# Kernel optimization log

Hardware: AMD Instinct MI355X
Metric: run time of the kernel (lower is better)

## Reference

```python
import jax, jax.numpy as jnp
import numpy as np

B, S, D, H = 2, 2048, 1024, 16
DK = D // H


def setup_inputs() -> dict:
    key = jax.random.key(0)
    ks = jax.random.split(key, 12)
    s = 1.0 / np.sqrt(D)
    return {
        "query": jax.random.normal(ks[0], (B, S, D), dtype=jnp.float32),
        "key": jax.random.normal(ks[1], (B, S, D), dtype=jnp.float32),
        "value": jax.random.normal(ks[2], (B, S, D), dtype=jnp.float32),
        "mask": jax.random.randint(ks[3], (B, 1, 1, S), 0, 2, dtype=jnp.int32),
        "wq": jax.random.normal(ks[4], (D, D), dtype=jnp.float32) * s,
        "bq": jnp.zeros((D,), dtype=jnp.float32),
        "wk": jax.random.normal(ks[5], (D, D), dtype=jnp.float32) * s,
        "bk": jnp.zeros((D,), dtype=jnp.float32),
        "wv": jax.random.normal(ks[6], (D, D), dtype=jnp.float32) * s,
        "bv": jnp.zeros((D,), dtype=jnp.float32),
        "wo": jax.random.normal(ks[7], (D, D), dtype=jnp.float32) * s,
        "bo": jnp.zeros((D,), dtype=jnp.float32),
    }


def reference(query, key, value, mask, wq, bq, wk, bk, wv, bv, wo, bo):
    b, s, d = query.shape
    # torch Linear: y = x @ W^T + b, then split heads -> [B, H, S, dk]
    def proj(x, w, bias):
        return (x @ w.T + bias).reshape(b, -1, H, DK).transpose(0, 2, 1, 3)

    q = proj(query, wq, bq)
    k = proj(key, wk, bk)
    v = proj(value, wv, bv)

    scores = jnp.einsum("bhqd,bhkd->bhqk", q, k) / jnp.sqrt(jnp.float32(DK))
    scores = jnp.where(mask == 0, jnp.float32(-1e9), scores)
    attn = jax.nn.softmax(scores, axis=-1)  # [B,H,S,S]
    x = jnp.einsum("bhqk,bhkd->bhqd", attn, v)
    x = x.transpose(0, 2, 1, 3).reshape(b, s, d)
    return x @ wo.T + bo
```

## Files before the change

kernel.cpp:

```cpp
#include <hip/hip_runtime.h>
#include <math.h>

#define B_  2
#define S_  2048
#define D_  1024
#define H_  16
#define DK_ 64

typedef unsigned short u16;
typedef unsigned int u32;
typedef __bf16 bf16x8 __attribute__((ext_vector_type(8)));
typedef float f32x4 __attribute__((ext_vector_type(4)));
typedef float f32x16 __attribute__((ext_vector_type(16)));
typedef u32 u32x2 __attribute__((ext_vector_type(2)));
typedef u32 u32x4 __attribute__((ext_vector_type(4)));

typedef const __attribute__((address_space(1))) void* gas1_t;
typedef __attribute__((address_space(3))) void* las3_t;

__device__ __forceinline__ void gload_lds16(const void* g, void* l) {
    __builtin_amdgcn_global_load_lds((gas1_t)g, (las3_t)l, 16, 0, 0);
}

__device__ __forceinline__ u16 f2bf(float f) {
    union { float f; unsigned u; } v; v.f = f;
    return (u16)((v.u + 0x7fffu + ((v.u >> 16) & 1u)) >> 16);
}

__device__ __forceinline__ u32 pack_bf16_2(float lo, float hi) {
    union { float f; u32 u; } a, b;
    a.f = lo; b.f = hi;
    return __builtin_amdgcn_perm(b.u + 0x8000u, a.u + 0x8000u, 0x07060302u);
}

__global__ __launch_bounds__(256)
void cast_all(const float* __restrict__ q, const float* __restrict__ k,
              const float* __restrict__ v, const float* __restrict__ wq,
              const float* __restrict__ wk, const float* __restrict__ wv,
              const float* __restrict__ wo, const int* __restrict__ mask,
              u16* __restrict__ qb, u16* __restrict__ kb, u16* __restrict__ vb,
              u16* __restrict__ wqb, u16* __restrict__ wkb, u16* __restrict__ wvb,
              u16* __restrict__ wob, float* __restrict__ mfac,
              float* __restrict__ nmaskf)
{
    const int bi = blockIdx.x;
    const int tid = threadIdx.x;
    if (bi >= 2064) {
        const int b = bi - 2064;
        __shared__ int red[256];
        int c = 0;
#pragma unroll
        for (int j = 0; j < 8; ++j)
            c += (mask[b * S_ + tid * 8 + j] == 0) ? 1 : 0;
        red[tid] = c;
        __syncthreads();
        for (int s = 128; s > 0; s >>= 1) {
            if (tid < s) red[tid] += red[tid + s];
            __syncthreads();
        }
        if (tid == 0) nmaskf[b] = (float)red[0];
        return;
    }
    if (bi >= 2048) {
        const int idx = (bi - 2048) * 256 + tid;
        mfac[idx] = mask[idx] ? 1.0f : 0.0f;
        return;
    }
#pragma unroll
    for (int j = 0; j < 8; ++j) {
        const int i = bi * 256 + tid + j * 524288;
        const float* src; u16* dst; int off;
        if (i < 3 * 1048576) {
            const int seg = i >> 20; off = i & 1048575;
            src = (seg == 0) ? q : (seg == 1) ? k : v;
            dst = (seg == 0) ? qb : (seg == 1) ? kb : vb;
        } else {
            const int jj = i - 3 * 1048576;
            const int seg = jj >> 18; off = jj & 262143;
            src = (seg == 0) ? wq : (seg == 1) ? wk : (seg == 2) ? wv : wo;
            dst = (seg == 0) ? wqb : (seg == 1) ? wkb : (seg == 2) ? wvb : wob;
        }
        const float4 val = ((const float4*)src)[off];
        uint2 o;
        o.x = pack_bf16_2(val.x, val.y);
        o.y = pack_bf16_2(val.z, val.w);
        ((uint2*)dst)[off] = o;
    }
}

template<int BN>
__device__ __forceinline__ void gemm_body(
    const u16* __restrict__ A, const u16* __restrict__ W,
    const float* __restrict__ bias, void* __restrict__ outp,
    float scale, int mode, int m0, int n0,
    const float* __restrict__ rowfac, const float* __restrict__ colfac)
{
    constexpr int NJ = BN / 32;
    __shared__ u16 sA[128 * 64];
    __shared__ u16 sW[BN * 64];

    const int tid  = threadIdx.x;
    const int wave = tid >> 6, lane = tid & 63;
    const int quad = lane >> 4, l16 = lane & 15;
    const int wm = (wave >> 1) * 64;
    const int wn = (wave & 1) * (BN / 2);
    const int srow = lane >> 3;
    const int scol = ((lane & 7) ^ srow) * 8;
    const int sw7  = l16 & 7;

    f32x4 acc[4][NJ];
    const f32x4 zero = {0.f, 0.f, 0.f, 0.f};
#pragma unroll
    for (int i = 0; i < 4; ++i)
#pragma unroll
        for (int j = 0; j < NJ; ++j) acc[i][j] = zero;

    const u16* ast = A + (size_t)(m0 + wave * 8 + srow) * D_ + scol;
    const u16* wst = W + (size_t)(n0 + wave * 8 + srow) * D_ + scol;

    for (int k0 = 0; k0 < D_; k0 += 64) {
#pragma unroll
        for (int t = 0; t < 4; ++t)
            gload_lds16(ast + (size_t)t * 32 * D_ + k0, sA + (wave + t * 4) * 512);
        if (BN == 128) {
#pragma unroll
            for (int t = 0; t < 4; ++t)
                gload_lds16(wst + (size_t)t * 32 * D_ + k0, sW + (wave + t * 4) * 512);
        } else {
#pragma unroll
            for (int t = 0; t < 2; ++t)
                gload_lds16(wst + (size_t)t * 32 * D_ + k0, sW + (wave + t * 4) * 512);
        }
        __syncthreads();

#pragma unroll
        for (int kh = 0; kh < 2; ++kh) {
            const int phys = ((kh * 4 + quad) ^ sw7) * 8;
            bf16x8 af[4], bfr[NJ];
#pragma unroll
            for (int i = 0; i < 4; ++i)
                af[i] = *(const bf16x8*)(sA + (wm + i * 16 + l16) * 64 + phys);
#pragma unroll
            for (int j = 0; j < NJ; ++j)
                bfr[j] = *(const bf16x8*)(sW + (wn + j * 16 + l16) * 64 + phys);
#pragma unroll
            for (int i = 0; i < 4; ++i)
#pragma unroll
                for (int j = 0; j < NJ; ++j)
                    acc[i][j] = __builtin_amdgcn_mfma_f32_16x16x32_bf16(af[i], bfr[j], acc[i][j], 0, 0, 0);
        }
        __syncthreads();
    }

#pragma unroll
    for (int i = 0; i < 4; ++i) {
        float rf4[4];
        if (mode == 1 && rowfac) {
#pragma unroll
            for (int r = 0; r < 4; ++r)
                rf4[r] = rowfac[m0 + wm + i * 16 + quad * 4 + r];
        }
#pragma unroll
        for (int j = 0; j < NJ; ++j) {
            const int n = n0 + wn + j * 16 + l16;
            if (mode == 3) {
                const float cf = colfac ? colfac[n] : 1.0f;
#pragma unroll
                for (int r = 0; r < 4; ++r) {
                    const int mp = m0 + wm + i * 16 + quad * 4 + r;
                    ((u16*)outp)[(size_t)mp * (B_ * S_) + n] = f2bf((acc[i][j][r] + bias[mp]) * cf);
                }
            } else {
                const float bn = bias[n];
#pragma unroll
                for (int r = 0; r < 4; ++r) {
                    const int m = m0 + wm + i * 16 + quad * 4 + r;
                    float v = acc[i][j][r] + bn;
                    if (mode == 0) {
                        ((float*)outp)[(size_t)m * D_ + n] = v;
                    } else {
                        v *= scale;
                        if (rowfac) v *= rf4[r];
                        const int b = m >> 11, s = m & (S_ - 1);
                        const int h = n >> 6, dk = n & 63;
                        ((u16*)outp)[(((size_t)(b * H_ + h)) * S_ + s) * DK_ + dk] = f2bf(v);
                    }
                }
            }
        }
    }
}

__global__ __launch_bounds__(256)
void qkv_gemm(const u16* __restrict__ qin, const u16* __restrict__ kin, const u16* __restrict__ vin,
              const u16* __restrict__ wqb, const u16* __restrict__ wkb, const u16* __restrict__ wvb,
              const float* __restrict__ bq, const float* __restrict__ bk, const float* __restrict__ bv,
              u16* __restrict__ Qp, u16* __restrict__ Kp, u16* __restrict__ Vt,
              const float* __restrict__ mfac)
{
    const int z = blockIdx.z;
    if (z == 2) {
        gemm_body<128>(wvb, vin, bv, Vt, 1.0f, 3, blockIdx.x * 128, blockIdx.y * 128,
                       nullptr, mfac);
    } else {
        const u16* A = (z == 0) ? qin : kin;
        const u16* W = (z == 0) ? wqb : wkb;
        const float* bias = (z == 0) ? bq : bk;
        u16* outp = (z == 0) ? Qp : Kp;
        const float scale = (z == 0) ? 0.18033688011112042f : 1.0f;
        const float* rf = (z == 1) ? mfac : nullptr;
        gemm_body<128>(A, W, bias, outp, scale, 1, blockIdx.y * 128, blockIdx.x * 128,
                       rf, nullptr);
    }
}

__global__ __launch_bounds__(256)
void out_gemm(const u16* __restrict__ Xc, const u16* __restrict__ wob,
              const float* __restrict__ bo, float* __restrict__ out)
{
    gemm_body<64>(Xc, wob, bo, out, 1.0f, 0, blockIdx.y * 128, blockIdx.x * 64,
                  nullptr, nullptr);
}

__global__ __launch_bounds__(512, 4)
void attn_mfma(const u16* __restrict__ Qp, const u16* __restrict__ Kp,
               const u16* __restrict__ Vt, const float* __restrict__ nmaskf,
               u16* __restrict__ Xc)
{
    __shared__ u16 sQ[128 * 64];
    __shared__ u16 sKVraw[16384];

    const int tid  = threadIdx.x;
    const int wave = tid >> 6, lane = tid & 63;
    const int qg = wave & 3, kg = wave >> 2;
    const int l31 = lane & 31, hi = lane >> 5;
    const int qt = blockIdx.x & 15;
    const int bh = blockIdx.x >> 4;
    const int b  = bh >> 4;
    const int h  = bh & 15;
    const int lr  = lane >> 3;
    const int cl  = (lane & 7) ^ lr;
    const int sw5 = l31 & 7;

    const u16* Qb = Qp + ((size_t)bh * S_ + qt * 128) * DK_;
    const u16* Kb = Kp + (size_t)bh * S_ * DK_;
    const int vdk = (qg * 8 + lr) + 32 * (cl >> 2);
    const u16* Vsrc = Vt + (size_t)(h * 64 + vdk) * (B_ * S_) + b * S_ + (cl & 3) * 8;
    const u16* Ksrc = Kb + (size_t)(qg * 8 + lr) * DK_ + cl * 8;

#pragma unroll
    for (int t = 0; t < 2; ++t)
        gload_lds16(Qb + (size_t)(wave * 16 + t * 8 + lr) * DK_ + cl * 8,
                    sQ + (wave * 2 + t) * 512);
    gload_lds16(Ksrc + (size_t)kg * 32 * DK_, sKVraw + (kg * 2) * 4096 + qg * 512);
    gload_lds16(Vsrc + kg * 32, sKVraw + (kg * 2) * 4096 + 2048 + qg * 512);
    __syncthreads();

    bf16x8 qf[4];
#pragma unroll
    for (int ks = 0; ks < 4; ++ks) {
        const int row = qg * 32 + l31;
        const int phys = (ks * 2 + hi) ^ sw5;
        qf[ks] = *(const bf16x8*)(sQ + row * 64 + phys * 8);
    }

    f32x16 oc[2];
    const f32x16 z16 = {0.f,0.f,0.f,0.f,0.f,0.f,0.f,0.f,
                        0.f,0.f,0.f,0.f,0.f,0.f,0.f,0.f};
    oc[0] = z16; oc[1] = z16;
    float lsum = 0.f;

    const u16* kpre = Ksrc + (size_t)(kg + 2) * 32 * DK_;
    const u16* vpre = Vsrc + (kg + 2) * 32;

    for (int i = 0; i < 32; ++i) {
        __syncthreads();
        const int cur = i & 1;

        if (i < 31) {
            u16* dst = sKVraw + (kg * 2 + (cur ^ 1)) * 4096;
            gload_lds16(kpre, dst + qg * 512);
            gload_lds16(vpre, dst + 2048 + qg * 512);
            kpre += (size_t)2 * 32 * DK_;
            vpre += 64;
        }
        const u16* sK = sKVraw + (kg * 2 + cur) * 4096;
        const u16* sV = sK + 2048;

        f32x16 sfr;
        {
            const bf16x8 k0 = *(const bf16x8*)(sK + l31 * 64 + (((0 * 2 + hi) ^ sw5)) * 8);
            const bf16x8 k1 = *(const bf16x8*)(sK + l31 * 64 + (((1 * 2 + hi) ^ sw5)) * 8);
            const bf16x8 k2 = *(const bf16x8*)(sK + l31 * 64 + (((2 * 2 + hi) ^ sw5)) * 8);
            const bf16x8 k3 = *(const bf16x8*)(sK + l31 * 64 + (((3 * 2 + hi) ^ sw5)) * 8);
            __builtin_amdgcn_s_setprio(1);
            sfr = __builtin_amdgcn_mfma_f32_32x32x16_bf16(k0, qf[0], z16, 0, 0, 0);
            sfr = __builtin_amdgcn_mfma_f32_32x32x16_bf16(k1, qf[1], sfr, 0, 0, 0);
            sfr = __builtin_amdgcn_mfma_f32_32x32x16_bf16(k2, qf[2], sfr, 0, 0, 0);
            sfr = __builtin_amdgcn_mfma_f32_32x32x16_bf16(k3, qf[3], sfr, 0, 0, 0);
            __builtin_amdgcn_s_setprio(0);
        }

        float p[16];
#pragma unroll
        for (int r = 0; r < 16; ++r) p[r] = __builtin_amdgcn_exp2f(sfr[r]);

        {
            const float s0 = (p[0] + p[1]) + (p[2] + p[3]);
            const float s1 = (p[4] + p[5]) + (p[6] + p[7]);
            const float s2 = (p[8] + p[9]) + (p[10] + p[11]);
            const float s3 = (p[12] + p[13]) + (p[14] + p[15]);
            lsum += (s0 + s1) + (s2 + s3);
        }

        const u32 W00 = pack_bf16_2(p[0], p[1]);
        const u32 W01 = pack_bf16_2(p[2], p[3]);
        const u32 W10 = pack_bf16_2(p[4], p[5]);
        const u32 W11 = pack_bf16_2(p[6], p[7]);
        const u32 W20 = pack_bf16_2(p[8], p[9]);
        const u32 W21 = pack_bf16_2(p[10], p[11]);
        const u32 W30 = pack_bf16_2(p[12], p[13]);
        const u32 W31 = pack_bf16_2(p[14], p[15]);

        const u32x2 s0 = __builtin_amdgcn_permlane32_swap(W00, W10, false, false);
        const u32x2 s1 = __builtin_amdgcn_permlane32_swap(W01, W11, false, false);
        const u32x2 s2 = __builtin_amdgcn_permlane32_swap(W20, W30, false, false);
        const u32x2 s3 = __builtin_amdgcn_permlane32_swap(W21, W31, false, false);
        u32x4 A0 = { s0[0], s1[0], s0[1], s1[1] };
        u32x4 A1 = { s2[0], s3[0], s2[1], s3[1] };
        const bf16x8 pa0 = *(const bf16x8*)&A0;
        const bf16x8 pa1 = *(const bf16x8*)&A1;

        {
            const bf16x8 v00 = *(const bf16x8*)(sV + l31 * 64 + (((0 + 0 + hi) ^ sw5)) * 8);
            const bf16x8 v01 = *(const bf16x8*)(sV + l31 * 64 + (((0 + 2 + hi) ^ sw5)) * 8);
            const bf16x8 v10 = *(const bf16x8*)(sV + l31 * 64 + (((4 + 0 + hi) ^ sw5)) * 8);
            const bf16x8 v11 = *(const bf16x8*)(sV + l31 * 64 + (((4 + 2 + hi) ^ sw5)) * 8);
            __builtin_amdgcn_s_setprio(1);
            oc[0] = __builtin_amdgcn_mfma_f32_32x32x16_bf16(pa0, v00, oc[0], 0, 0, 0);
            oc[0] = __builtin_amdgcn_mfma_f32_32x32x16_bf16(pa1, v01, oc[0], 0, 0, 0);
            oc[1] = __builtin_amdgcn_mfma_f32_32x32x16_bf16(pa0, v10, oc[1], 0, 0, 0);
            oc[1] = __builtin_amdgcn_mfma_f32_32x32x16_bf16(pa1, v11, oc[1], 0, 0, 0);
            __builtin_amdgcn_s_setprio(0);
        }
    }

    {
        union { float f; u32 u; } lu; lu.f = lsum;
        const u32x2 lr2 = __builtin_amdgcn_permlane32_swap(lu.u, lu.u, false, false);
        union { u32 u; float f; } pu; pu.u = hi ? lr2[0] : lr2[1];
        lsum += pu.f;
    }

    __syncthreads();
    float* sL = (float*)sQ;
    float* sO = (float*)sKVraw;
    if (hi == 0) sL[kg * 128 + qg * 32 + l31] = lsum;
    if (kg == 1) {
#pragma unroll
        for (int dh = 0; dh < 2; ++dh)
#pragma unroll
            for (int g = 0; g < 4; ++g) {
                f32x4 t = { oc[dh][g * 4 + 0], oc[dh][g * 4 + 1],
                            oc[dh][g * 4 + 2], oc[dh][g * 4 + 3] };
                *(f32x4*)(sO + qg * 2048 + ((dh * 4 + g) * 2 + hi) * 128 + l31 * 4) = t;
            }
    }
    __syncthreads();
    if (kg == 0) {
        const float nm = nmaskf[b];
#pragma unroll
        for (int g = 0; g < 4; ++g) {
            const f32x4 oA = *(const f32x4*)(sO + qg * 2048 + ((0 + g) * 2 + hi) * 128 + l31 * 4);
            const f32x4 oB = *(const f32x4*)(sO + qg * 2048 + ((4 + g) * 2 + hi) * 128 + l31 * 4);
#pragma unroll
            for (int rr = 0; rr < 4; ++rr) {
                const int qrow = rr + 8 * g + 4 * hi;
                const float inv = __builtin_amdgcn_rcpf(
                    sL[qg * 32 + qrow] + sL[128 + qg * 32 + qrow] - nm);
                const int s = qt * 128 + qg * 32 + qrow;
                const size_t base = ((size_t)(b * S_ + s)) * D_ + h * 64 + l31;
                Xc[base]      = f2bf((oc[0][g * 4 + rr] + oA[rr]) * inv);
                Xc[base + 32] = f2bf((oc[1][g * 4 + rr] + oB[rr]) * inv);
            }
        }
    }
}

extern "C" void kernel_launch(void* const* d_in, const int* in_sizes, int n_in,
                              void* d_out, int out_size, void* d_ws, size_t ws_size,
                              hipStream_t stream)
{
    (void)in_sizes; (void)n_in; (void)out_size; (void)ws_size;

    const float* query = (const float*)d_in[0];
    const float* key   = (const float*)d_in[1];
    const float* value = (const float*)d_in[2];
    const int*   mask  = (const int*)d_in[3];
    const float* wq    = (const float*)d_in[4];
    const float* bq    = (const float*)d_in[5];
    const float* wk    = (const float*)d_in[6];
    const float* bk    = (const float*)d_in[7];
    const float* wv    = (const float*)d_in[8];
    const float* bv    = (const float*)d_in[9];
    const float* wo    = (const float*)d_in[10];
    const float* bo    = (const float*)d_in[11];

    const size_t NE = (size_t)B_ * S_ * D_;
    const size_t WE = (size_t)D_ * D_;

    u16* qb  = (u16*)d_ws;
    u16* kb  = qb + NE;
    u16* vb  = kb + NE;
    u16* wqb = vb + NE;
    u16* wkb = wqb + WE;
    u16* wvb = wkb + WE;
    u16* wob = wvb + WE;
    u16* Qp  = wob + WE;
    u16* Kp  = Qp + NE;
    u16* Vt  = Kp + NE;
    float* mfac   = (float*)(Vt + NE);
    float* nmaskf = mfac + 4096;
    u16* Xc  = qb;

    cast_all<<<2066, 256, 0, stream>>>(query, key, value, wq, wk, wv, wo, mask,
                                       qb, kb, vb, wqb, wkb, wvb, wob, mfac, nmaskf);

    qkv_gemm<<<dim3(D_ / 128, (B_ * S_) / 128, 3), 256, 0, stream>>>(
        qb, kb, vb, wqb, wkb, wvb, bq, bk, bv, Qp, Kp, Vt, mfac);

    attn_mfma<<<dim3(B_ * H_ * (S_ / 128)), 512, 0, stream>>>(Qp, Kp, Vt, nmaskf, Xc);

    out_gemm<<<dim3(D_ / 64, (B_ * S_) / 128), 256, 0, stream>>>(Xc, wob, bo, (float*)d_out);
}
```

Before: 221.0 us.

## Process two K/V tiles per attention iteration and load Q directly to registers

The attention loop now stages two 32-key K/V sub-tiles per wave group in each double-buffered stage. This halves the iteration count and barrier count, and interleaves two independent QK^T MFMA chains so their latency is hidden. Q fragments are read straight from global memory into registers instead of through LDS, and probabilities are packed with the hardware v_cvt_pk_bf16_f32 instruction rather than a manual rounding perm. The cost is more registers and doubled LDS (64KB) per block, which may reduce occupancy under the 512-thread, 4-block launch bound.

```diff
diff --git a/kernel.cpp b/kernel.cpp
--- a/kernel.cpp
+++ b/kernel.cpp
@@ -31,6 +31,12 @@
     union { float f; u32 u; } a, b;
     a.f = lo; b.f = hi;
     return __builtin_amdgcn_perm(b.u + 0x8000u, a.u + 0x8000u, 0x07060302u);
+}
+
+__device__ __forceinline__ u32 cvtpk_bf16(float lo, float hi) {
+    u32 r;
+    asm("v_cvt_pk_bf16_f32 %0, %1, %2" : "=v"(r) : "v"(lo), "v"(hi));
+    return r;
 }
 
 __global__ __launch_bounds__(256)
@@ -227,8 +233,7 @@
                const u16* __restrict__ Vt, const float* __restrict__ nmaskf,
                u16* __restrict__ Xc)
 {
-    __shared__ u16 sQ[128 * 64];
-    __shared__ u16 sKVraw[16384];
+    __shared__ u16 sKV[2][2][8192];
 
     const int tid  = threadIdx.x;
     const int wave = tid >> 6, lane = tid & 63;
@@ -248,20 +253,25 @@
     const u16* Vsrc = Vt + (size_t)(h * 64 + vdk) * (B_ * S_) + b * S_ + (cl & 3) * 8;
     const u16* Ksrc = Kb + (size_t)(qg * 8 + lr) * DK_ + cl * 8;
 
-#pragma unroll
-    for (int t = 0; t < 2; ++t)
-        gload_lds16(Qb + (size_t)(wave * 16 + t * 8 + lr) * DK_ + cl * 8,
-                    sQ + (wave * 2 + t) * 512);
-    gload_lds16(Ksrc + (size_t)kg * 32 * DK_, sKVraw + (kg * 2) * 4096 + qg * 512);
-    gload_lds16(Vsrc + kg * 32, sKVraw + (kg * 2) * 4096 + 2048 + qg * 512);
-    __syncthreads();
-
     bf16x8 qf[4];
-#pragma unroll
-    for (int ks = 0; ks < 4; ++ks) {
-        const int row = qg * 32 + l31;
-        const int phys = (ks * 2 + hi) ^ sw5;
-        qf[ks] = *(const bf16x8*)(sQ + row * 64 + phys * 8);
+    {
+        const u16* qrow = Qb + (size_t)(qg * 32 + l31) * DK_ + hi * 8;
+        qf[0] = *(const bf16x8*)(qrow);
+        qf[1] = *(const bf16x8*)(qrow + 16);
+        qf[2] = *(const bf16x8*)(qrow + 32);
+        qf[3] = *(const bf16x8*)(qrow + 48);
+    }
+
+    const u16* kpre = Ksrc + (size_t)kg * 64 * DK_;
+    const u16* vpre = Vsrc + kg * 64;
+    {
+        u16* dst = sKV[kg][0];
+        gload_lds16(kpre,                    dst + qg * 512);
+        gload_lds16(kpre + (size_t)32 * DK_, dst + 2048 + qg * 512);
+        gload_lds16(vpre,                    dst + 4096 + qg * 512);
+        gload_lds16(vpre + 32,               dst + 6144 + qg * 512);
+        kpre += (size_t)128 * DK_;
+        vpre += 128;
     }
 
     f32x16 oc[2];
@@ -270,76 +280,116 @@
     oc[0] = z16; oc[1] = z16;
     float lsum = 0.f;
 
-    const u16* kpre = Ksrc + (size_t)(kg + 2) * 32 * DK_;
-    const u16* vpre = Vsrc + (kg + 2) * 32;
-
-    for (int i = 0; i < 32; ++i) {
+    for (int i = 0; i < 16; ++i) {
         __syncthreads();
         const int cur = i & 1;
 
-        if (i < 31) {
-            u16* dst = sKVraw + (kg * 2 + (cur ^ 1)) * 4096;
-            gload_lds16(kpre, dst + qg * 512);
-            gload_lds16(vpre, dst + 2048 + qg * 512);
-            kpre += (size_t)2 * 32 * DK_;
-            vpre += 64;
-        }
-        const u16* sK = sKVraw + (kg * 2 + cur) * 4096;
-        const u16* sV = sK + 2048;
-
-        f32x16 sfr;
+        if (i < 15) {
+            u16* dst = sKV[kg][cur ^ 1];
+            gload_lds16(kpre,                    dst + qg * 512);
+            gload_lds16(kpre + (size_t)32 * DK_, dst + 2048 + qg * 512);
+            gload_lds16(vpre,                    dst + 4096 + qg * 512);
+            gload_lds16(vpre + 32,               dst + 6144 + qg * 512);
+            kpre += (size_t)128 * DK_;
+            vpre += 128;
+        }
+        const u16* sKA = sKV[kg][cur];
+        const u16* sKB = sKA + 2048;
+        const u16* sVA = sKA + 4096;
+        const u16* sVB = sKA + 6144;
+
+        f32x16 sfrA, sfrB;
         {
-            const bf16x8 k0 = *(const bf16x8*)(sK + l31 * 64 + (((0 * 2 + hi) ^ sw5)) * 8);
-            const bf16x8 k1 = *(const bf16x8*)(sK + l31 * 64 + (((1 * 2 + hi) ^ sw5)) * 8);
-            const bf16x8 k2 = *(const bf16x8*)(sK + l31 * 64 + (((2 * 2 + hi) ^ sw5)) * 8);
-            const bf16x8 k3 = *(const bf16x8*)(sK + l31 * 64 + (((3 * 2 + hi) ^ sw5)) * 8);
+            const bf16x8 a0 = *(const bf16x8*)(sKA + l31 * 64 + (((0 + hi) ^ sw5)) * 8);
+            const bf16x8 a1 = *(const bf16x8*)(sKA + l31 * 64 + (((2 + hi) ^ sw5)) * 8);
+            const bf16x8 a2 = *(const bf16x8*)(sKA + l31 * 64 + (((4 + hi) ^ sw5)) * 8);
+            const bf16x8 a3 = *(const bf16x8*)(sKA + l31 * 64 + (((6 + hi) ^ sw5)) * 8);
+            const bf16x8 b0 = *(const bf16x8*)(sKB + l31 * 64 + (((0 + hi) ^ sw5)) * 8);
+            const bf16x8 b1 = *(const bf16x8*)(sKB + l31 * 64 + (((2 + hi) ^ sw5)) * 8);
+            const bf16x8 b2 = *(const bf16x8*)(sKB + l31 * 64 + (((4 + hi) ^ sw5)) * 8);
+            const bf16x8 b3 = *(const bf16x8*)(sKB + l31 * 64 + (((6 + hi) ^ sw5)) * 8);
             __builtin_amdgcn_s_setprio(1);
-            sfr = __builtin_amdgcn_mfma_f32_32x32x16_bf16(k0, qf[0], z16, 0, 0, 0);
-            sfr = __builtin_amdgcn_mfma_f32_32x32x16_bf16(k1, qf[1], sfr, 0, 0, 0);
-            sfr = __builtin_amdgcn_mfma_f32_32x32x16_bf16(k2, qf[2], sfr, 0, 0, 0);
-            sfr = __builtin_amdgcn_mfma_f32_32x32x16_bf16(k3, qf[3], sfr, 0, 0, 0);
+            sfrA = __builtin_amdgcn_mfma_f32_32x32x16_bf16(a0, qf[0], z16, 0, 0, 0);
+            sfrB = __builtin_amdgcn_mfma_f32_32x32x16_bf16(b0, qf[0], z16, 0, 0, 0);
+            sfrA = __builtin_amdgcn_mfma_f32_32x32x16_bf16(a1, qf[1], sfrA, 0, 0, 0);
+            sfrB = __builtin_amdgcn_mfma_f32_32x32x16_bf16(b1, qf[1], sfrB, 0, 0, 0);
+            sfrA = __builtin_amdgcn_mfma_f32_32x32x16_bf16(a2, qf[2], sfrA, 0, 0, 0);
+            sfrB = __builtin_amdgcn_mfma_f32_32x32x16_bf16(b2, qf[2], sfrB, 0, 0, 0);
+            sfrA = __builtin_amdgcn_mfma_f32_32x32x16_bf16(a3, qf[3], sfrA, 0, 0, 0);
+            sfrB = __builtin_amdgcn_mfma_f32_32x32x16_bf16(b3, qf[3], sfrB, 0, 0, 0);
             __builtin_amdgcn_s_setprio(0);
         }
 
-        float p[16];
-#pragma unroll
-        for (int r = 0; r < 16; ++r) p[r] = __builtin_amdgcn_exp2f(sfr[r]);
-
         {
+            float p[16];
+#pragma unroll
+            for (int r = 0; r < 16; ++r) p[r] = __builtin_amdgcn_exp2f(sfrA[r]);
             const float s0 = (p[0] + p[1]) + (p[2] + p[3]);
             const float s1 = (p[4] + p[5]) + (p[6] + p[7]);
             const float s2 = (p[8] + p[9]) + (p[10] + p[11]);
             const float s3 = (p[12] + p[13]) + (p[14] + p[15]);
             lsum += (s0 + s1) + (s2 + s3);
-        }
-
-        const u32 W00 = pack_bf16_2(p[0], p[1]);
-        const u32 W01 = pack_bf16_2(p[2], p[3]);
-        const u32 W10 = pack_bf16_2(p[4], p[5]);
-        const u32 W11 = pack_bf16_2(p[6], p[7]);
-        const u32 W20 = pack_bf16_2(p[8], p[9]);
-        const u32 W21 = pack_bf16_2(p[10], p[11]);
-        const u32 W30 = pack_bf16_2(p[12], p[13]);
-        const u32 W31 = pack_bf16_2(p[14], p[15]);
-
-        const u32x2 s0 = __builtin_amdgcn_permlane32_swap(W00, W10, false, false);
-        const u32x2 s1 = __builtin_amdgcn_permlane32_swap(W01, W11, false, false);
-        const u32x2 s2 = __builtin_amdgcn_permlane32_swap(W20, W30, false, false);
-        const u32x2 s3 = __builtin_amdgcn_permlane32_swap(W21, W31, false, false);
-        u32x4 A0 = { s0[0], s1[0], s0[1], s1[1] };
-        u32x4 A1 = { s2[0], s3[0], s2[1], s3[1] };
-        const bf16x8 pa0 = *(const bf16x8*)&A0;
-        const bf16x8 pa1 = *(const bf16x8*)&A1;
-
-        {
-            const bf16x8 v00 = *(const bf16x8*)(sV + l31 * 64 + (((0 + 0 + hi) ^ sw5)) * 8);
-            const bf16x8 v01 = *(const bf16x8*)(sV + l31 * 64 + (((0 + 2 + hi) ^ sw5)) * 8);
-            const bf16x8 v10 = *(const bf16x8*)(sV + l31 * 64 + (((4 + 0 + hi) ^ sw5)) * 8);
-            const bf16x8 v11 = *(const bf16x8*)(sV + l31 * 64 + (((4 + 2 + hi) ^ sw5)) * 8);
+            const u32 W00 = cvtpk_bf16(p[0], p[1]);
+            const u32 W01 = cvtpk_bf16(p[2], p[3]);
+            const u32 W10 = cvtpk_bf16(p[4], p[5]);
+            const u32 W11 = cvtpk_bf16(p[6], p[7]);
+            const u32 W20 = cvtpk_bf16(p[8], p[9]);
+            const u32 W21 = cvtpk_bf16(p[10], p[11]);
+            const u32 W30 = cvtpk_bf16(p[12], p[13]);
+            const u32 W31 = cvtpk_bf16(p[14], p[15]);
+            const u32x2 e0 = __builtin_amdgcn_permlane32_swap(W00, W10, false, false);
+            const u32x2 e1 = __builtin_amdgcn_permlane32_swap(W01, W11, false, false);
+            const u32x2 e2 = __builtin_amdgcn_permlane32_swap(W20, W30, false, false);
+            const u32x2 e3 = __builtin_amdgcn_permlane32_swap(W21, W31, false, false);
+            u32x4 A0 = { e0[0], e1[0], e0[1], e1[1] };
+            u32x4 A1 = { e2[0], e3[0], e2[1], e3[1] };
+            const bf16x8 pa0 = *(const bf16x8*)&A0;
+            const bf16x8 pa1 = *(const bf16x8*)&A1;
+            const bf16x8 v00 = *(const bf16x8*)(sVA + l31 * 64 + (((0 + hi) ^ sw5)) * 8);
+            const bf16x8 v01 = *(const bf16x8*)(sVA + l31 * 64 + (((2 + hi) ^ sw5)) * 8);
+            const bf16x8 v10 = *(const bf16x8*)(sVA + l31 * 64 + (((4 + hi) ^ sw5)) * 8);
+            const bf16x8 v11 = *(const bf16x8*)(sVA + l31 * 64 + (((6 + hi) ^ sw5)) * 8);
             __builtin_amdgcn_s_setprio(1);
             oc[0] = __builtin_amdgcn_mfma_f32_32x32x16_bf16(pa0, v00, oc[0], 0, 0, 0);
+            oc[1] = __builtin_amdgcn_mfma_f32_32x32x16_bf16(pa0, v10, oc[1], 0, 0, 0);
             oc[0] = __builtin_amdgcn_mfma_f32_32x32x16_bf16(pa1, v01, oc[0], 0, 0, 0);
+            oc[1] = __builtin_amdgcn_mfma_f32_32x32x16_bf16(pa1, v11, oc[1], 0, 0, 0);
+            __builtin_amdgcn_s_setprio(0);
+        }
+
+        {
+            float p[16];
+#pragma unroll
+            for (int r = 0; r < 16; ++r) p[r] = __builtin_amdgcn_exp2f(sfrB[r]);
+            const float s0 = (p[0] + p[1]) + (p[2] + p[3]);
+            const float s1 = (p[4] + p[5]) + (p[6] + p[7]);
+            const float s2 = (p[8] + p[9]) + (p[10] + p[11]);
+            const float s3 = (p[12] + p[13]) + (p[14] + p[15]);
+            lsum += (s0 + s1) + (s2 + s3);
+            const u32 W00 = cvtpk_bf16(p[0], p[1]);
+            const u32 W01 = cvtpk_bf16(p[2], p[3]);
+            const u32 W10 = cvtpk_bf16(p[4], p[5]);
+            const u32 W11 = cvtpk_bf16(p[6], p[7]);
+            const u32 W20 = cvtpk_bf16(p[8], p[9]);
+            const u32 W21 = cvtpk_bf16(p[10], p[11]);
+            const u32 W30 = cvtpk_bf16(p[12], p[13]);
+            const u32 W31 = cvtpk_bf16(p[14], p[15]);
+            const u32x2 e0 = __builtin_amdgcn_permlane32_swap(W00, W10, false, false);
+            const u32x2 e1 = __builtin_amdgcn_permlane32_swap(W01, W11, false, false);
+            const u32x2 e2 = __builtin_amdgcn_permlane32_swap(W20, W30, false, false);
+            const u32x2 e3 = __builtin_amdgcn_permlane32_swap(W21, W31, false, false);
+            u32x4 A0 = { e0[0], e1[0], e0[1], e1[1] };
+            u32x4 A1 = { e2[0], e3[0], e2[1], e3[1] };
+            const bf16x8 pa0 = *(const bf16x8*)&A0;
+            const bf16x8 pa1 = *(const bf16x8*)&A1;
+            const bf16x8 v00 = *(const bf16x8*)(sVB + l31 * 64 + (((0 + hi) ^ sw5)) * 8);
+            const bf16x8 v01 = *(const bf16x8*)(sVB + l31 * 64 + (((2 + hi) ^ sw5)) * 8);
+            const bf16x8 v10 = *(const bf16x8*)(sVB + l31 * 64 + (((4 + hi) ^ sw5)) * 8);
+            const bf16x8 v11 = *(const bf16x8*)(sVB + l31 * 64 + (((6 + hi) ^ sw5)) * 8);
+            __builtin_amdgcn_s_setprio(1);
+            oc[0] = __builtin_amdgcn_mfma_f32_32x32x16_bf16(pa0, v00, oc[0], 0, 0, 0);
             oc[1] = __builtin_amdgcn_mfma_f32_32x32x16_bf16(pa0, v10, oc[1], 0, 0, 0);
+            oc[0] = __builtin_amdgcn_mfma_f32_32x32x16_bf16(pa1, v01, oc[0], 0, 0, 0);
             oc[1] = __builtin_amdgcn_mfma_f32_32x32x16_bf16(pa1, v11, oc[1], 0, 0, 0);
             __builtin_amdgcn_s_setprio(0);
         }
@@ -353,8 +403,8 @@
     }
 
     __syncthreads();
-    float* sL = (float*)sQ;
-    float* sO = (float*)sKVraw;
+    float* sO = (float*)&sKV[0][0][0];
+    float* sL = (float*)((char*)sO + 32768);
     if (hi == 0) sL[kg * 128 + qg * 32 + l31] = lsum;
     if (kg == 1) {
 #pragma unroll
```

After: 221.0 us. No clear change (+0.0%).
